# Performance work log

Measured on AMD Instinct MI355X. Metric: run time of the kernel, lower is better.

The kernel has to match this reference:

```python
import jax, jax.numpy as jnp
import numpy as np

V, T, NS, NH, E, H = 4, 4, 100000, 12288, 100000, 64
NEG_SLOPE = 0.01  # nn.LeakyReLU default


def setup_inputs() -> dict:
    key = jax.random.key(0)
    k1, k2, k3, k4, k5 = jax.random.split(key, 5)
    x = jax.random.normal(k1, (V, T, NS), dtype=jnp.float32)          # per-var, per-t scalar node features
    src_idx = jax.random.randint(k2, (V, T, E), 0, NS, dtype=jnp.int32)
    dst_idx = jax.random.randint(k3, (V, T, E), 0, NH, dtype=jnp.int32)
    W = jax.random.normal(k4, (V, T, H), dtype=jnp.float32)            # GraphConv weight, in_feats=1 -> [1,H] per etype
    b = jax.random.normal(k5, (V, T, H), dtype=jnp.float32) * 0.02     # GraphConv bias per etype
    return {"x": x, "W": W, "b": b, "src_idx": src_idx, "dst_idx": dst_idx, "n_healpix": NH}


def reference(x, W, b, src_idx, dst_idx, n_healpix):
    # x: [V,T,NS]; W,b: [V,T,H]; src_idx,dst_idx: [V,T,E]
    x = jnp.nan_to_num(x, nan=0.0)

    def conv_scalar(x_v, src, dst):
        # x_v: [T,NS] (all timestep features for this var), src/dst: [E] for ONE edge type
        ones = jnp.ones(src.shape, x_v.dtype)
        deg_out = jax.ops.segment_sum(ones, src, num_segments=NS)       # out-degree of src nodes
        deg_in = jax.ops.segment_sum(ones, dst, num_segments=n_healpix)  # in-degree of dst nodes
        norm_src = jax.lax.rsqrt(jnp.maximum(deg_out, 1.0))
        norm_dst = jax.lax.rsqrt(jnp.maximum(deg_in, 1.0))
        msg = x_v[:, src] * norm_src[src]                                # [T,E] gather
        agg = jax.vmap(lambda m: jax.ops.segment_sum(m, dst, num_segments=n_healpix))(msg)  # [T,NH]
        return agg * norm_dst                                            # norm='both'

    # HeteroGraphConv bug-faithful: for each var, EVERY per-t' conv is applied to each x[:,t]
    # s[v, t', t, n] = normalized scatter of x[v,t] through edges of etype t'
    s = jax.vmap(lambda xv, sv, dv: jax.vmap(lambda se, de: conv_scalar(xv, se, de))(sv, dv))(
        x, src_idx, dst_idx)                                             # [V,T',T,NH]

    # in_feats=1: linear is outer product with W row; bias + LeakyReLU inside each conv, sum over etypes t'
    h = jax.nn.leaky_relu(s[..., None] * W[:, :, None, None, :] + b[:, :, None, None, :],
                          negative_slope=NEG_SLOPE)                      # [V,T',T,NH,H]
    out = h.sum(axis=1)                                                  # aggregate='sum' over edge types -> [V,T,NH,H]
    # final stacking: stack over t (dim=1) then over vars (dim=1) -> [NH, V, T, H]
    return jnp.transpose(out, (2, 0, 1, 3))
```

## Files before the change

kernel.cpp:

```cpp
#include <hip/hip_runtime.h>
#include <math.h>

#define V    4
#define T    4
#define NSRC 100000
#define NHX  12288
#define E    100000
#define H    64
#define VT   16
#define NP   5

#define DQ   4
#define DR   (NHX/DQ)
#define DRP  (DR+1)
#define SC   4
#define SE   (E/SC)

#define RCH   4
#define RBINS (NSRC/RCH)
#define RW    (RBINS/2)
#define HF    4
#define HE    (E/HF)

#define NPB  8

__global__ void transpose_kernel(const float* __restrict__ x,
                                 float4* __restrict__ x4) {
    const int v = blockIdx.y;
    const int s = blockIdx.x * 256 + threadIdx.x;
    if (s >= NSRC) return;
    const float* xr = x + (size_t)v * T * NSRC + s;
    float a0 = xr[0], a1 = xr[NSRC], a2 = xr[2 * NSRC], a3 = xr[3 * NSRC];
    float4 r;
    r.x = (a0 == a0) ? a0 : 0.0f;
    r.y = (a1 == a1) ? a1 : 0.0f;
    r.z = (a2 == a2) ? a2 : 0.0f;
    r.w = (a3 == a3) ? a3 : 0.0f;
    x4[(size_t)v * NSRC + s] = r;
}

__global__ void __launch_bounds__(1024)
cnt_kernel(const int* __restrict__ src, unsigned int* __restrict__ cnt_part) {
    const int rg = blockIdx.x, hf = blockIdx.y, vt = blockIdx.z;
    const int lo = rg * RBINS;
    __shared__ unsigned int pack[RW];
    for (int i = threadIdx.x; i < RW; i += 1024) pack[i] = 0u;
    __syncthreads();
    const int* s_row = src + vt * E + hf * HE;
    for (int e = threadIdx.x; e < HE; e += 1024) {
        const unsigned r = (unsigned)(s_row[e] - lo);
        if (r < RBINS) atomicAdd(&pack[r >> 1], 1u << ((r & 1) * 16));
    }
    __syncthreads();
    unsigned int* outp = cnt_part + ((size_t)hf * VT + vt) * (NSRC / 2) + rg * RW;
    for (int i = threadIdx.x; i < RW; i += 1024) outp[i] = pack[i];
}

__global__ void nsfin_kernel(const unsigned int* __restrict__ cnt_part,
                             float2* __restrict__ ns2) {
    const size_t w = (size_t)blockIdx.x * 256 + threadIdx.x;
    unsigned c = 0;
#pragma unroll
    for (int hf = 0; hf < HF; ++hf)
        c += cnt_part[(size_t)hf * VT * (NSRC / 2) + w];
    float2 r;
    r.x = rsqrtf(fmaxf((float)(c & 0xFFFFu), 1.0f));
    r.y = rsqrtf(fmaxf((float)(c >> 16), 1.0f));
    ns2[w] = r;
}

__global__ void __launch_bounds__(1024)
scatter_kernel(const float4* __restrict__ x4, const int* __restrict__ src,
               const int* __restrict__ dst, const float* __restrict__ ns,
               float* __restrict__ part) {
    const int b  = blockIdx.x;
    const int k  = b & 7;
    const int j  = b >> 3;
    const int vt = 2 * k + (j & 1);
    const int r2 = j >> 1;
    const int dq = r2 & 3;
    const int c  = r2 >> 2;
    const int v  = vt >> 2;
    const int dlo = dq * DR;

    __shared__ float agg[NP * DRP];
    for (int i = threadIdx.x; i < NP * DRP; i += 1024) agg[i] = 0.0f;
    __syncthreads();

    const int*    s_row  = src + vt * E + c * SE;
    const int*    d_row  = dst + vt * E + c * SE;
    const float*  ns_row = ns + (size_t)vt * NSRC;
    const float4* x_row  = x4 + (size_t)v * NSRC;
    for (int e = threadIdx.x; e < SE; e += 1024) {
        const int s = s_row[e];
        const unsigned r = (unsigned)(d_row[e] - dlo);
        if (r < DR) {
            const float4 xv = x_row[s];
            const float  nv = ns_row[s];
            atomicAdd(&agg[0 * DRP + r], xv.x * nv);
            atomicAdd(&agg[1 * DRP + r], xv.y * nv);
            atomicAdd(&agg[2 * DRP + r], xv.z * nv);
            atomicAdd(&agg[3 * DRP + r], xv.w * nv);
            atomicAdd(&agg[4 * DRP + r], 1.0f);
        }
    }
    __syncthreads();

    float* base = part + ((size_t)(c * VT + vt) * NP) * NHX + dlo;
    for (int i = threadIdx.x; i < NP * DR; i += 1024) {
        const int p = i / DR, q = i - p * DR;
        base[(size_t)p * NHX + q] = agg[p * DRP + q];
    }
}

__global__ void epilogue_kernel(const float* __restrict__ part,
                                const float* __restrict__ Wm,
                                const float* __restrict__ bm,
                                float* __restrict__ out) {
    const int n0  = blockIdx.x * NPB;
    const int tid = threadIdx.x;
    __shared__ float sW[VT * H];
    __shared__ float sb[VT * H];
    __shared__ float sraw[VT][NP][NPB];
    __shared__ float sv[VT][T][NPB];

    for (int i = tid; i < VT * H; i += 256) { sW[i] = Wm[i]; sb[i] = bm[i]; }
    for (int w = tid; w < VT * NP * NPB; w += 256) {
        const int n  = w & (NPB - 1);
        const int p  = (w >> 3) % NP;
        const int vt = w / (NP * NPB);
        float s = 0.0f;
#pragma unroll
        for (int c = 0; c < SC; ++c)
            s += part[(((size_t)(c * VT + vt)) * NP + p) * NHX + n0 + n];
        sraw[vt][p][n] = s;
    }
    __syncthreads();
    for (int w = tid; w < VT * T * NPB; w += 256) {
        const int n  = w & (NPB - 1);
        const int t  = (w >> 3) & 3;
        const int vt = w >> 5;
        sv[vt][t][n] = sraw[vt][t][n] * rsqrtf(fmaxf(sraw[vt][NP - 1][n], 1.0f));
    }
    __syncthreads();

    const int v  = tid >> 6;
    const int t  = (tid >> 4) & 3;
    const int hb = (tid & 15) * 4;
    float4 Wr[4], Br[4];
#pragma unroll
    for (int tp = 0; tp < 4; ++tp) {
        const int wi = (v * 4 + tp) * H + hb;
        Wr[tp] = *(const float4*)&sW[wi];
        Br[tp] = *(const float4*)&sb[wi];
    }
#pragma unroll
    for (int n = 0; n < NPB; ++n) {
        float4 o = make_float4(0.f, 0.f, 0.f, 0.f);
#pragma unroll
        for (int tp = 0; tp < 4; ++tp) {
            const float s = sv[v * 4 + tp][t][n];
            float a;
            a = fmaf(s, Wr[tp].x, Br[tp].x); o.x += (a > 0.f) ? a : 0.01f * a;
            a = fmaf(s, Wr[tp].y, Br[tp].y); o.y += (a > 0.f) ? a : 0.01f * a;
            a = fmaf(s, Wr[tp].z, Br[tp].z); o.z += (a > 0.f) ? a : 0.01f * a;
            a = fmaf(s, Wr[tp].w, Br[tp].w); o.w += (a > 0.f) ? a : 0.01f * a;
        }
        ((float4*)(out + (size_t)(n0 + n) * (V * T * H)))[tid] = o;
    }
}

extern "C" void kernel_launch(void* const* d_in, const int* in_sizes, int n_in,
                              void* d_out, int out_size, void* d_ws, size_t ws_size,
                              hipStream_t stream) {
    const float* x   = (const float*)d_in[0];
    const float* Wm  = (const float*)d_in[1];
    const float* bm  = (const float*)d_in[2];
    const int*   src = (const int*)d_in[3];
    const int*   dst = (const int*)d_in[4];
    float* out = (float*)d_out;

    char* ws = (char*)d_ws;
    float4* x4 = (float4*)ws;
    size_t off = (size_t)V * NSRC * sizeof(float4);
    float* ns = (float*)(ws + off);
    off += (size_t)VT * NSRC * sizeof(float);
    float* part = (float*)(ws + off);
    unsigned int* cnt_part = (unsigned int*)(ws + off);

    transpose_kernel<<<dim3((NSRC + 255) / 256, V), 256, 0, stream>>>(x, x4);
    cnt_kernel<<<dim3(RCH, HF, VT), 1024, 0, stream>>>(src, cnt_part);
    nsfin_kernel<<<(VT * (NSRC / 2)) / 256, 256, 0, stream>>>(cnt_part, (float2*)ns);
    scatter_kernel<<<DQ * SC * VT, 1024, 0, stream>>>(x4, src, dst, ns, part);
    epilogue_kernel<<<NHX / NPB, 256, 0, stream>>>(part, Wm, bm, out);
}
```

Measured before the change: 169.2 us.

## Pack degree counts into 8-bit bins, widen grids, and unroll scatter loop by two

The degree-count kernel now packs four 8-bit counters per word, so each block covers half the source range with twice the bins, and the edge list is split into 16 slices instead of 4. The finalize kernel unpacks the four bytes and writes float4 norms per vt. The scatter kernel splits edges into 8 chunks instead of 4 and handles two edges per thread per iteration, so gathers can be in flight before the LDS atomics. The goal is more blocks on the GPU and more memory-level parallelism. The cost is more partial buffers for the epilogue to sum, and 8-bit counters that could overflow if one slice holds more than 255 edges to the same source.

Result: slower. 174.7 us (+3.3%).

```diff
diff --git a/kernel.cpp b/kernel.cpp
--- a/kernel.cpp
+++ b/kernel.cpp
@@ -13,13 +13,13 @@
 #define DQ   4
 #define DR   (NHX/DQ)
 #define DRP  (DR+1)
-#define SC   4
+#define SC   8
 #define SE   (E/SC)
 
-#define RCH   4
+#define RCH   2
 #define RBINS (NSRC/RCH)
-#define RW    (RBINS/2)
-#define HF    4
+#define RW    (RBINS/4)
+#define HF    16
 #define HE    (E/HF)
 
 #define NPB  8
@@ -49,24 +49,31 @@
     const int* s_row = src + vt * E + hf * HE;
     for (int e = threadIdx.x; e < HE; e += 1024) {
         const unsigned r = (unsigned)(s_row[e] - lo);
-        if (r < RBINS) atomicAdd(&pack[r >> 1], 1u << ((r & 1) * 16));
-    }
-    __syncthreads();
-    unsigned int* outp = cnt_part + ((size_t)hf * VT + vt) * (NSRC / 2) + rg * RW;
+        if (r < RBINS) atomicAdd(&pack[r >> 2], 1u << ((r & 3) * 8));
+    }
+    __syncthreads();
+    unsigned int* outp = cnt_part + ((size_t)hf * VT + vt) * (NSRC / 4) + rg * RW;
     for (int i = threadIdx.x; i < RW; i += 1024) outp[i] = pack[i];
 }
 
 __global__ void nsfin_kernel(const unsigned int* __restrict__ cnt_part,
-                             float2* __restrict__ ns2) {
-    const size_t w = (size_t)blockIdx.x * 256 + threadIdx.x;
-    unsigned c = 0;
-#pragma unroll
-    for (int hf = 0; hf < HF; ++hf)
-        c += cnt_part[(size_t)hf * VT * (NSRC / 2) + w];
-    float2 r;
-    r.x = rsqrtf(fmaxf((float)(c & 0xFFFFu), 1.0f));
-    r.y = rsqrtf(fmaxf((float)(c >> 16), 1.0f));
-    ns2[w] = r;
+                             float4* __restrict__ ns4) {
+    const int vt = blockIdx.y;
+    const int wd = blockIdx.x * 256 + threadIdx.x;
+    if (wd >= NSRC / 4) return;
+    unsigned c0 = 0, c1 = 0, c2 = 0, c3 = 0;
+#pragma unroll
+    for (int hf = 0; hf < HF; ++hf) {
+        const unsigned w = cnt_part[((size_t)hf * VT + vt) * (NSRC / 4) + wd];
+        c0 += w & 0xFFu; c1 += (w >> 8) & 0xFFu;
+        c2 += (w >> 16) & 0xFFu; c3 += w >> 24;
+    }
+    float4 r;
+    r.x = rsqrtf(fmaxf((float)c0, 1.0f));
+    r.y = rsqrtf(fmaxf((float)c1, 1.0f));
+    r.z = rsqrtf(fmaxf((float)c2, 1.0f));
+    r.w = rsqrtf(fmaxf((float)c3, 1.0f));
+    ns4[(size_t)vt * (NSRC / 4) + wd] = r;
 }
 
 __global__ void __launch_bounds__(1024)
@@ -91,17 +98,33 @@
     const int*    d_row  = dst + vt * E + c * SE;
     const float*  ns_row = ns + (size_t)vt * NSRC;
     const float4* x_row  = x4 + (size_t)v * NSRC;
-    for (int e = threadIdx.x; e < SE; e += 1024) {
-        const int s = s_row[e];
-        const unsigned r = (unsigned)(d_row[e] - dlo);
-        if (r < DR) {
-            const float4 xv = x_row[s];
-            const float  nv = ns_row[s];
-            atomicAdd(&agg[0 * DRP + r], xv.x * nv);
-            atomicAdd(&agg[1 * DRP + r], xv.y * nv);
-            atomicAdd(&agg[2 * DRP + r], xv.z * nv);
-            atomicAdd(&agg[3 * DRP + r], xv.w * nv);
-            atomicAdd(&agg[4 * DRP + r], 1.0f);
+
+    for (int e = threadIdx.x; e < SE; e += 2048) {
+        const int eB = e + 1024;
+        const int sA = s_row[e];
+        const unsigned rA = (unsigned)(d_row[e] - dlo);
+        int sB = 0; unsigned rB = 0xFFFFFFFFu;
+        if (eB < SE) { sB = s_row[eB]; rB = (unsigned)(d_row[eB] - dlo); }
+
+        float4 xA; float nA = 0.0f;
+        float4 xB; float nB = 0.0f;
+        const bool okA = rA < DR, okB = rB < DR;
+        if (okA) { xA = x_row[sA]; nA = ns_row[sA]; }
+        if (okB) { xB = x_row[sB]; nB = ns_row[sB]; }
+
+        if (okA) {
+            atomicAdd(&agg[0 * DRP + rA], xA.x * nA);
+            atomicAdd(&agg[1 * DRP + rA], xA.y * nA);
+            atomicAdd(&agg[2 * DRP + rA], xA.z * nA);
+            atomicAdd(&agg[3 * DRP + rA], xA.w * nA);
+            atomicAdd(&agg[4 * DRP + rA], 1.0f);
+        }
+        if (okB) {
+            atomicAdd(&agg[0 * DRP + rB], xB.x * nB);
+            atomicAdd(&agg[1 * DRP + rB], xB.y * nB);
+            atomicAdd(&agg[2 * DRP + rB], xB.z * nB);
+            atomicAdd(&agg[3 * DRP + rB], xB.w * nB);
+            atomicAdd(&agg[4 * DRP + rB], 1.0f);
         }
     }
     __syncthreads();
@@ -190,7 +213,7 @@
 
     transpose_kernel<<<dim3((NSRC + 255) / 256, V), 256, 0, stream>>>(x, x4);
     cnt_kernel<<<dim3(RCH, HF, VT), 1024, 0, stream>>>(src, cnt_part);
-    nsfin_kernel<<<(VT * (NSRC / 2)) / 256, 256, 0, stream>>>(cnt_part, (float2*)ns);
+    nsfin_kernel<<<dim3((NSRC / 4 + 255) / 256, VT), 256, 0, stream>>>(cnt_part, (float4*)ns);
     scatter_kernel<<<DQ * SC * VT, 1024, 0, stream>>>(x4, src, dst, ns, part);
     epilogue_kernel<<<NHX / NPB, 256, 0, stream>>>(part, Wm, bm, out);
 }
```

## Replace shared-memory atomic scatter with CSR sort-by-destination and gather accumulation

Applied to the files above, without the earlier changes.

Replaces the destination-partitioned shared-atomic scatter with a counting sort of edges by destination: per-slice histograms, a prefix-scan kernel, a reorder kernel, then one thread per destination accumulates its incoming edges without float atomics. The source-degree count moves to 8-bit packed bins in a single kernel that also writes the rsqrt norms, which drops the separate finalize pass. This removes repeated full edge-list passes per destination quarter and the float atomic contention, at the cost of more kernel launches, a serial-ish scan, and unbalanced per-thread loops when in-degrees vary. The 8-bit packing assumes no source has out-degree of 256 or more.

Result: slower. 218.1 us (+28.9%).

```diff
diff --git a/kernel.cpp b/kernel.cpp
--- a/kernel.cpp
+++ b/kernel.cpp
@@ -8,20 +8,12 @@
 #define E    100000
 #define H    64
 #define VT   16
-#define NP   5
-
-#define DQ   4
-#define DR   (NHX/DQ)
-#define DRP  (DR+1)
-#define SC   4
-#define SE   (E/SC)
-
-#define RCH   4
+
+#define SL   8
+#define SLE  (E/SL)
+#define RCH  2
 #define RBINS (NSRC/RCH)
-#define RW    (RBINS/2)
-#define HF    4
-#define HE    (E/HF)
-
+#define RW   (RBINS/4)
 #define NPB  8
 
 __global__ void transpose_kernel(const float* __restrict__ x,
@@ -40,80 +32,149 @@
 }
 
 __global__ void __launch_bounds__(1024)
-cnt_kernel(const int* __restrict__ src, unsigned int* __restrict__ cnt_part) {
-    const int rg = blockIdx.x, hf = blockIdx.y, vt = blockIdx.z;
+ns_kernel(const int* __restrict__ src, float* __restrict__ ns) {
+    const int rg = blockIdx.x, vt = blockIdx.y;
     const int lo = rg * RBINS;
     __shared__ unsigned int pack[RW];
     for (int i = threadIdx.x; i < RW; i += 1024) pack[i] = 0u;
     __syncthreads();
-    const int* s_row = src + vt * E + hf * HE;
-    for (int e = threadIdx.x; e < HE; e += 1024) {
+    const int* s_row = src + vt * E;
+    for (int e = threadIdx.x; e < E; e += 1024) {
         const unsigned r = (unsigned)(s_row[e] - lo);
-        if (r < RBINS) atomicAdd(&pack[r >> 1], 1u << ((r & 1) * 16));
-    }
-    __syncthreads();
-    unsigned int* outp = cnt_part + ((size_t)hf * VT + vt) * (NSRC / 2) + rg * RW;
-    for (int i = threadIdx.x; i < RW; i += 1024) outp[i] = pack[i];
-}
-
-__global__ void nsfin_kernel(const unsigned int* __restrict__ cnt_part,
-                             float2* __restrict__ ns2) {
-    const size_t w = (size_t)blockIdx.x * 256 + threadIdx.x;
-    unsigned c = 0;
-#pragma unroll
-    for (int hf = 0; hf < HF; ++hf)
-        c += cnt_part[(size_t)hf * VT * (NSRC / 2) + w];
-    float2 r;
-    r.x = rsqrtf(fmaxf((float)(c & 0xFFFFu), 1.0f));
-    r.y = rsqrtf(fmaxf((float)(c >> 16), 1.0f));
-    ns2[w] = r;
-}
-
-__global__ void __launch_bounds__(1024)
-scatter_kernel(const float4* __restrict__ x4, const int* __restrict__ src,
-               const int* __restrict__ dst, const float* __restrict__ ns,
-               float* __restrict__ part) {
-    const int b  = blockIdx.x;
-    const int k  = b & 7;
-    const int j  = b >> 3;
+        if (r < RBINS) atomicAdd(&pack[r >> 2], 1u << ((r & 3) * 8));
+    }
+    __syncthreads();
+    float4* nsp = (float4*)(ns + (size_t)vt * NSRC + lo);
+    for (int w = threadIdx.x; w < RW; w += 1024) {
+        const unsigned u = pack[w];
+        float4 r4;
+        r4.x = rsqrtf(fmaxf((float)(u & 0xFFu), 1.0f));
+        r4.y = rsqrtf(fmaxf((float)((u >> 8) & 0xFFu), 1.0f));
+        r4.z = rsqrtf(fmaxf((float)((u >> 16) & 0xFFu), 1.0f));
+        r4.w = rsqrtf(fmaxf((float)(u >> 24), 1.0f));
+        nsp[w] = r4;
+    }
+}
+
+__global__ void __launch_bounds__(1024)
+dhist_kernel(const int* __restrict__ dst, unsigned int* __restrict__ ph) {
+    const int sl = blockIdx.x, vt = blockIdx.y;
+    __shared__ unsigned int h[NHX];
+    for (int i = threadIdx.x; i < NHX; i += 1024) h[i] = 0u;
+    __syncthreads();
+    const int* d_row = dst + vt * E + sl * SLE;
+    for (int e = threadIdx.x; e < SLE; e += 1024)
+        atomicAdd(&h[d_row[e]], 1u);
+    __syncthreads();
+    unsigned int* outp = ph + ((size_t)vt * SL + sl) * NHX;
+    for (int i = threadIdx.x; i < NHX; i += 1024) outp[i] = h[i];
+}
+
+__global__ void __launch_bounds__(1024)
+dscan_kernel(const unsigned int* __restrict__ ph,
+             unsigned int* __restrict__ start,
+             unsigned int* __restrict__ colstart,
+             unsigned int* __restrict__ degs,
+             float* __restrict__ ndst) {
+    const int vt   = blockIdx.x;
+    const int tid  = threadIdx.x;
+    const int lane = tid & 63, wv = tid >> 6;
+    __shared__ unsigned int wsum[16];
+    __shared__ unsigned int running;
+    if (tid == 0) running = 0u;
+    __syncthreads();
+    for (int ch = 0; ch < NHX / 1024; ++ch) {
+        const int d = ch * 1024 + tid;
+        unsigned int h[SL];
+        unsigned int tot = 0;
+#pragma unroll
+        for (int s = 0; s < SL; ++s) {
+            h[s] = ph[((size_t)vt * SL + s) * NHX + d];
+            tot += h[s];
+        }
+        unsigned int incl = tot;
+#pragma unroll
+        for (int off = 1; off < 64; off <<= 1) {
+            const unsigned int vup = (unsigned int)__shfl_up((int)incl, off, 64);
+            if (lane >= off) incl += vup;
+        }
+        if (lane == 63) wsum[wv] = incl;
+        __syncthreads();
+        if (tid == 0) {
+            unsigned int r = running;
+#pragma unroll
+            for (int w = 0; w < 16; ++w) { const unsigned int t2 = wsum[w]; wsum[w] = r; r += t2; }
+            running = r;
+        }
+        __syncthreads();
+        const unsigned int base = wsum[wv] + (incl - tot);
+        colstart[(size_t)vt * NHX + d] = base;
+        degs[(size_t)vt * NHX + d]     = tot;
+        ndst[(size_t)vt * NHX + d]     = rsqrtf(fmaxf((float)tot, 1.0f));
+        unsigned int acc = base;
+#pragma unroll
+        for (int s = 0; s < SL; ++s) {
+            start[((size_t)vt * SL + s) * NHX + d] = acc;
+            acc += h[s];
+        }
+        __syncthreads();
+    }
+}
+
+__global__ void __launch_bounds__(1024)
+reorder_kernel(const int* __restrict__ src, const int* __restrict__ dst,
+               const unsigned int* __restrict__ start,
+               int* __restrict__ sorted) {
+    const int sl = blockIdx.x, vt = blockIdx.y;
+    __shared__ unsigned int pos[NHX];
+    const unsigned int* st = start + ((size_t)vt * SL + sl) * NHX;
+    for (int i = threadIdx.x; i < NHX; i += 1024) pos[i] = st[i];
+    __syncthreads();
+    const int* s_row = src + vt * E + sl * SLE;
+    const int* d_row = dst + vt * E + sl * SLE;
+    int* outp = sorted + (size_t)vt * E;
+    for (int e = threadIdx.x; e < SLE; e += 1024) {
+        const int d = d_row[e];
+        const int s = s_row[e];
+        const unsigned int p = atomicAdd(&pos[d], 1u);
+        outp[p] = s;
+    }
+}
+
+__global__ void __launch_bounds__(256)
+accum_kernel(const float4* __restrict__ x4, const int* __restrict__ sorted,
+             const float* __restrict__ ns,
+             const unsigned int* __restrict__ colstart,
+             const unsigned int* __restrict__ degs,
+             const float* __restrict__ ndst,
+             float4* __restrict__ sval) {
+    const int b = blockIdx.x;
+    const int k = b & 7;
+    const int j = b >> 3;
     const int vt = 2 * k + (j & 1);
-    const int r2 = j >> 1;
-    const int dq = r2 & 3;
-    const int c  = r2 >> 2;
-    const int v  = vt >> 2;
-    const int dlo = dq * DR;
-
-    __shared__ float agg[NP * DRP];
-    for (int i = threadIdx.x; i < NP * DRP; i += 1024) agg[i] = 0.0f;
-    __syncthreads();
-
-    const int*    s_row  = src + vt * E + c * SE;
-    const int*    d_row  = dst + vt * E + c * SE;
+    const int chunk = j >> 1;
+    const int d = chunk * 256 + threadIdx.x;
+    const int v = vt >> 2;
+    const size_t vd = (size_t)vt * NHX + d;
+    const unsigned int base = colstart[vd];
+    const unsigned int deg  = degs[vd];
+    const float nd = ndst[vd];
+    const int*    srt    = sorted + (size_t)vt * E;
     const float*  ns_row = ns + (size_t)vt * NSRC;
     const float4* x_row  = x4 + (size_t)v * NSRC;
-    for (int e = threadIdx.x; e < SE; e += 1024) {
-        const int s = s_row[e];
-        const unsigned r = (unsigned)(d_row[e] - dlo);
-        if (r < DR) {
-            const float4 xv = x_row[s];
-            const float  nv = ns_row[s];
-            atomicAdd(&agg[0 * DRP + r], xv.x * nv);
-            atomicAdd(&agg[1 * DRP + r], xv.y * nv);
-            atomicAdd(&agg[2 * DRP + r], xv.z * nv);
-            atomicAdd(&agg[3 * DRP + r], xv.w * nv);
-            atomicAdd(&agg[4 * DRP + r], 1.0f);
-        }
-    }
-    __syncthreads();
-
-    float* base = part + ((size_t)(c * VT + vt) * NP) * NHX + dlo;
-    for (int i = threadIdx.x; i < NP * DR; i += 1024) {
-        const int p = i / DR, q = i - p * DR;
-        base[(size_t)p * NHX + q] = agg[p * DRP + q];
-    }
-}
-
-__global__ void epilogue_kernel(const float* __restrict__ part,
+    float4 acc = make_float4(0.f, 0.f, 0.f, 0.f);
+    for (unsigned int i = 0; i < deg; ++i) {
+        const int s = srt[base + i];
+        const float4 xv = x_row[s];
+        const float  nv = ns_row[s];
+        acc.x += xv.x * nv; acc.y += xv.y * nv;
+        acc.z += xv.z * nv; acc.w += xv.w * nv;
+    }
+    acc.x *= nd; acc.y *= nd; acc.z *= nd; acc.w *= nd;
+    sval[vd] = acc;
+}
+
+__global__ void epilogue_kernel(const float4* __restrict__ sval,
                                 const float* __restrict__ Wm,
                                 const float* __restrict__ bm,
                                 float* __restrict__ out) {
@@ -121,26 +182,14 @@
     const int tid = threadIdx.x;
     __shared__ float sW[VT * H];
     __shared__ float sb[VT * H];
-    __shared__ float sraw[VT][NP][NPB];
     __shared__ float sv[VT][T][NPB];
 
     for (int i = tid; i < VT * H; i += 256) { sW[i] = Wm[i]; sb[i] = bm[i]; }
-    for (int w = tid; w < VT * NP * NPB; w += 256) {
-        const int n  = w & (NPB - 1);
-        const int p  = (w >> 3) % NP;
-        const int vt = w / (NP * NPB);
-        float s = 0.0f;
-#pragma unroll
-        for (int c = 0; c < SC; ++c)
-            s += part[(((size_t)(c * VT + vt)) * NP + p) * NHX + n0 + n];
-        sraw[vt][p][n] = s;
-    }
-    __syncthreads();
-    for (int w = tid; w < VT * T * NPB; w += 256) {
-        const int n  = w & (NPB - 1);
-        const int t  = (w >> 3) & 3;
-        const int vt = w >> 5;
-        sv[vt][t][n] = sraw[vt][t][n] * rsqrtf(fmaxf(sraw[vt][NP - 1][n], 1.0f));
+    if (tid < VT * NPB) {
+        const int vt = tid >> 3, n = tid & 7;
+        const float4 r = sval[(size_t)vt * NHX + n0 + n];
+        sv[vt][0][n] = r.x; sv[vt][1][n] = r.y;
+        sv[vt][2][n] = r.z; sv[vt][3][n] = r.w;
     }
     __syncthreads();
 
@@ -181,16 +230,22 @@
     float* out = (float*)d_out;
 
     char* ws = (char*)d_ws;
-    float4* x4 = (float4*)ws;
-    size_t off = (size_t)V * NSRC * sizeof(float4);
-    float* ns = (float*)(ws + off);
-    off += (size_t)VT * NSRC * sizeof(float);
-    float* part = (float*)(ws + off);
-    unsigned int* cnt_part = (unsigned int*)(ws + off);
+    size_t off = 0;
+    float4* x4 = (float4*)(ws + off);            off += (size_t)V * NSRC * sizeof(float4);
+    float4* sval = (float4*)(ws + off);          off += (size_t)VT * NHX * sizeof(float4);
+    float* ns = (float*)(ws + off);              off += (size_t)VT * NSRC * sizeof(float);
+    unsigned int* ph = (unsigned int*)(ws + off);       off += (size_t)VT * SL * NHX * 4;
+    unsigned int* start = (unsigned int*)(ws + off);    off += (size_t)VT * SL * NHX * 4;
+    unsigned int* colstart = (unsigned int*)(ws + off); off += (size_t)VT * NHX * 4;
+    unsigned int* degs = (unsigned int*)(ws + off);     off += (size_t)VT * NHX * 4;
+    float* ndst = (float*)(ws + off);                   off += (size_t)VT * NHX * 4;
+    int* sorted = (int*)(ws + off);                     off += (size_t)VT * E * 4;
 
     transpose_kernel<<<dim3((NSRC + 255) / 256, V), 256, 0, stream>>>(x, x4);
-    cnt_kernel<<<dim3(RCH, HF, VT), 1024, 0, stream>>>(src, cnt_part);
-    nsfin_kernel<<<(VT * (NSRC / 2)) / 256, 256, 0, stream>>>(cnt_part, (float2*)ns);
-    scatter_kernel<<<DQ * SC * VT, 1024, 0, stream>>>(x4, src, dst, ns, part);
-    epilogue_kernel<<<NHX / NPB, 256, 0, stream>>>(part, Wm, bm, out);
-}
+    ns_kernel<<<dim3(RCH, VT), 1024, 0, stream>>>(src, ns);
+    dhist_kernel<<<dim3(SL, VT), 1024, 0, stream>>>(dst, ph);
+    dscan_kernel<<<VT, 1024, 0, stream>>>(ph, start, colstart, degs, ndst);
+    reorder_kernel<<<dim3(SL, VT), 1024, 0, stream>>>(src, dst, start, sorted);
+    accum_kernel<<<768, 256, 0, stream>>>(x4, sorted, ns, colstart, degs, ndst, sval);
+    epilogue_kernel<<<NHX / NPB, 256, 0, stream>>>(sval, Wm, bm, out);
+}
```
